# Optimization experiments

Measured on AMD Instinct MI355X. Metric: run time of the kernel, lower is better.

## Reference

```python
import jax, jax.numpy as jnp
import numpy as np

CODEBOOK_SIZE = 8192
HIDDEN_SIZE = 256
N_ANCHORS = 5


def setup_inputs() -> dict:
    key = jax.random.key(0)
    k1, k2 = jax.random.split(key)
    z = jax.random.normal(k1, (8, 4096, HIDDEN_SIZE), dtype=jnp.float32)
    emb = 0.02 * jax.random.normal(k2, (CODEBOOK_SIZE, HIDDEN_SIZE), dtype=jnp.float32)
    # enforce_anchor_values(): first 5 rows are one-hot anchors (eye padded with zeros)
    anchors = jnp.zeros((N_ANCHORS, HIDDEN_SIZE), dtype=jnp.float32)
    anchors = anchors.at[:, :N_ANCHORS].set(jnp.eye(N_ANCHORS, dtype=jnp.float32))
    emb = emb.at[:N_ANCHORS, :].set(anchors)
    return {"z": z, "emb": emb}


def reference(z, emb):
    b, t, h = z.shape
    flat = z.reshape(b * t, h)
    # squared L2 distance: ||z||^2 - 2 z.e + ||e||^2  -> [b*t, K]
    dist = (
        jnp.sum(flat * flat, axis=1, keepdims=True)
        - 2.0 * (flat @ emb.T)
        + jnp.sum(emb * emb, axis=1)[None, :]
    )
    idx = jnp.argmin(dist, axis=1)  # [b*t]
    z_q = emb[idx].reshape(b, t, h)
    # straight-through estimator
    z_st = z + jax.lax.stop_gradient(z_q - z)
    codebook_loss = jnp.mean((z_q - jax.lax.stop_gradient(z)) ** 2)
    commit_loss = jnp.mean((z - jax.lax.stop_gradient(z_q)) ** 2)
    return z_st, idx.reshape(b, t), codebook_loss, commit_loss
```

## Files before the change

### kernel.cpp

```cpp
#include <hip/hip_runtime.h>

#define HIDDEN 256
#define K_CODES 8192
#define N_TOK 32768
#define ZST_ELEMS 8388608
#define N_ANCHORS 5
#define NCH 64
#define MARGIN 8.0e-3f
#define WLS_CAP 131072
#define WLC_CAP 131072
#define EPI_BLOCKS 8192

using short8 = __attribute__((ext_vector_type(8))) short;
using f32x4  = __attribute__((ext_vector_type(4))) float;

__device__ __forceinline__ unsigned short f2bf(float f) {
    unsigned int u = __float_as_uint(f);
    return (unsigned short)((u + 0x7fffu + ((u >> 16) & 1u)) >> 16);
}

__device__ __forceinline__ void gl2lds16(const void* g, void* l) {
    __builtin_amdgcn_global_load_lds(
        (const __attribute__((address_space(1))) unsigned int*)g,
        (__attribute__((address_space(3))) unsigned int*)l, 16, 0, 0);
}

__device__ __forceinline__ unsigned long long score_key(float s, int code) {
    unsigned int u = __float_as_uint(s);
    u = (u & 0x80000000u) ? ~u : (u | 0x80000000u);
    return (((unsigned long long)u) << 32) | (unsigned int)code;
}

__global__ void prep_kernel(const float* __restrict__ emb, const float* __restrict__ z,
                            float* __restrict__ ne, float* __restrict__ zn,
                            unsigned short* __restrict__ Bh, unsigned short* __restrict__ Ah) {
#pragma clang fp contract(off)
    int gt  = blockIdx.x * 256 + threadIdx.x;
    int row = gt >> 4;
    int sub = gt & 15;
    const float* src; unsigned short* dst; float* nrm;
    if (row < K_CODES) {
        src = emb + (size_t)row * HIDDEN;
        dst = Bh  + (size_t)row * HIDDEN;
        nrm = ne + row;
    } else {
        int r2 = row - K_CODES;
        src = z  + (size_t)r2 * HIDDEN;
        dst = Ah + (size_t)r2 * HIDDEN;
        nrm = zn + r2;
    }
    const float* p = src + (sub >> 3) * 128 + (sub & 7);
    float v = p[0];
    float r = v * v;
    #pragma unroll
    for (int i = 1; i < 16; ++i) { float w = p[8 * i]; r += w * w; }
    r += __shfl_xor(r, 1, 64);
    r += __shfl_xor(r, 2, 64);
    r += __shfl_xor(r, 4, 64);
    r += __shfl_xor(r, 8, 64);
    if (sub == 0) *nrm = r;

    const float4* s4 = (const float4*)src + sub * 4;
    #pragma unroll
    for (int j = 0; j < 2; ++j) {
        float4 a = s4[2 * j];
        float4 b = s4[2 * j + 1];
        short8 h;
        h[0] = (short)f2bf(a.x); h[1] = (short)f2bf(a.y);
        h[2] = (short)f2bf(a.z); h[3] = (short)f2bf(a.w);
        h[4] = (short)f2bf(b.x); h[5] = (short)f2bf(b.y);
        h[6] = (short)f2bf(b.z); h[7] = (short)f2bf(b.w);
        *(short8*)(dst + sub * 16 + j * 8) = h;
    }
}

__global__ __launch_bounds__(512, 4) void mfma_score_kernel(
    const unsigned short* __restrict__ Ah,
    const unsigned short* __restrict__ Bh,
    const float* __restrict__ ne,
    float* __restrict__ p1, float* __restrict__ p2, unsigned short* __restrict__ piu) {

    __shared__ unsigned short Ahs[3][256 * 32];
    __shared__ unsigned short Bhs[3][128 * 32];

    const int tid  = threadIdx.x;
    const int wm   = tid >> 6;
    const int lane = tid & 63;
    const int L    = lane & 15;
    const int q    = lane >> 4;

    const int lin  = blockIdx.x;
    const int xcd  = lin & 7;
    const int s    = lin >> 3;
    const int nb   = s >> 4;
    const int m0   = (xcd * 16 + (s & 15)) * 256;
    const int n0   = nb * 128;

    f32x4 acc[2][8] = {};

    auto STAGE = [&](int kt, int buf) {
        const int k0 = kt * 32;
        #pragma unroll
        for (int r = 0; r < 2; ++r) {
            int u   = tid + 512 * r;
            int row = u >> 2;
            int p   = u & 3;
            int ch  = p ^ ((row >> 1) & 3);
            gl2lds16(Ah + (size_t)(m0 + row) * HIDDEN + k0 + ch * 8,
                     &Ahs[buf][u * 8]);
        }
        {
            int u   = tid;
            int row = u >> 2;
            int p   = u & 3;
            int ch  = p ^ ((row >> 1) & 3);
            gl2lds16(Bh + (size_t)(n0 + row) * HIDDEN + k0 + ch * 8,
                     &Bhs[buf][u * 8]);
        }
    };

    STAGE(0, 0);
    STAGE(1, 1);
    asm volatile("s_waitcnt vmcnt(3)" ::: "memory");
    __builtin_amdgcn_s_barrier();
    asm volatile("" ::: "memory");

    #pragma unroll
    for (int kt = 0; kt < 8; ++kt) {
        const int cur = kt % 3;

        const short8* A8h = (const short8*)Ahs[cur];
        const short8* B8h = (const short8*)Bhs[cur];

        short8 ah[2];
        #pragma unroll
        for (int tm = 0; tm < 2; ++tm) {
            int m  = wm * 32 + tm * 16 + L;
            ah[tm] = A8h[m * 4 + (q ^ ((m >> 1) & 3))];
        }

        if (kt + 2 < 8) STAGE(kt + 2, (kt + 2) % 3);

        __builtin_amdgcn_s_setprio(1);
        #pragma unroll
        for (int tn = 0; tn < 8; ++tn) {
            int n  = tn * 16 + L;
            short8 bh = B8h[n * 4 + (q ^ ((n >> 1) & 3))];
            #pragma unroll
            for (int tm = 0; tm < 2; ++tm) {
                acc[tm][tn] = __builtin_amdgcn_mfma_f32_16x16x32_bf16(
                    ah[tm], bh, acc[tm][tn], 0, 0, 0);
            }
        }
        __builtin_amdgcn_s_setprio(0);

        asm volatile("" ::: "memory");
        __builtin_amdgcn_s_barrier();
        if (kt < 7) {
            if (kt < 6) asm volatile("s_waitcnt vmcnt(3)" ::: "memory");
            else        asm volatile("s_waitcnt vmcnt(0)" ::: "memory");
            __builtin_amdgcn_s_barrier();
            asm volatile("" ::: "memory");
        }
    }

    float nev[8];
    #pragma unroll
    for (int tn = 0; tn < 8; ++tn) nev[tn] = ne[n0 + tn * 16 + L];
    if (nb == 0 && L < N_ANCHORS) nev[0] = 3.4e38f;

    #pragma unroll
    for (int tm = 0; tm < 2; ++tm) {
        #pragma unroll
        for (int reg = 0; reg < 4; ++reg) {
            float m1 = 3.4e38f, m2 = 3.4e38f;
            int bi = 0;
            #pragma unroll
            for (int tn = 0; tn < 8; ++tn) {
                float s2 = nev[tn] - 2.0f * acc[tm][tn][reg];
                int lo = tn * 16 + L;
                if (s2 < m1)      { m2 = m1; m1 = s2; bi = lo; }
                else if (s2 < m2) { m2 = s2; }
            }
            #pragma unroll
            for (int off = 1; off < 16; off <<= 1) {
                float o1 = __shfl_xor(m1, off, 64);
                float o2 = __shfl_xor(m2, off, 64);
                int   oi = __shfl_xor(bi, off, 64);
                if (o1 < m1 || (o1 == m1 && oi < bi)) {
                    m2 = fminf(m1, o2); m1 = o1; bi = oi;
                } else {
                    m2 = fminf(m2, o1);
                }
            }
            if (L == 0) {
                size_t mrow = (size_t)m0 + wm * 32 + tm * 16 + q * 4 + reg;
                p1[(size_t)nb * N_TOK + mrow]  = m1;
                p2[(size_t)nb * N_TOK + mrow]  = m2;
                piu[(size_t)nb * N_TOK + mrow] = (unsigned short)bi;
            }
        }
    }
}

__global__ void combine_kernel(const float* __restrict__ p1, const float* __restrict__ p2,
                               const unsigned short* __restrict__ piu,
                               const float* __restrict__ z, const float* __restrict__ zn,
                               const float* __restrict__ ne,
                               float* __restrict__ idxf, int* __restrict__ flags,
                               unsigned long long* __restrict__ slots,
                               int* __restrict__ wls, int* __restrict__ wlc,
                               unsigned int* __restrict__ wcnt) {
#pragma clang fp contract(off)
    int gt  = blockIdx.x * 256 + threadIdx.x;
    int t   = gt >> 3;
    int sub = gt & 7;

    float o1v[8], o2v[8];
    float m1 = 3.4e38f, m2 = 3.4e38f;
    int bi = 0;
    #pragma unroll
    for (int j = 0; j < 8; ++j) {
        int nb = sub + j * 8;
        float o1 = p1[(size_t)nb * N_TOK + t];
        float o2 = p2[(size_t)nb * N_TOK + t];
        o1v[j] = o1; o2v[j] = o2;
        if (o1 < m1) {
            m2 = fminf(m1, o2); m1 = o1;
            bi = nb * 128 + (int)piu[(size_t)nb * N_TOK + t];
        } else {
            m2 = fminf(m2, o1);
        }
    }
    #pragma unroll
    for (int off = 1; off < 8; off <<= 1) {
        float o1 = __shfl_xor(m1, off, 64);
        float o2 = __shfl_xor(m2, off, 64);
        int   oi = __shfl_xor(bi, off, 64);
        if (o1 < m1 || (o1 == m1 && oi < bi)) {
            m2 = fminf(m1, o2); m1 = o1; bi = oi;
        } else {
            m2 = fminf(m2, o1);
        }
    }
    float zt = zn[t];
    const float* zp = z + (size_t)t * HIDDEN;
    float sa = 3.4e38f; int ai = 0;
    #pragma unroll
    for (int a = 0; a < N_ANCHORS; ++a) {
        float s = (zt - 2.0f * zp[a]) + ne[a];
        if (s < sa) { sa = s; ai = a; }
    }
    float g = sa - zt;
    bool anchorWin = (g + MARGIN < m1);
    bool amb = !anchorWin && ((m2 - m1 < MARGIN) || (g <= m1 + MARGIN));
    if (sub == 0) {
        slots[t] = score_key(sa, ai);
        idxf[t]  = anchorWin ? (float)ai : (float)bi;
        flags[t] = amb ? 1 : 0;
    }
    if (amb) {
        float thr = m1 + MARGIN;
        #pragma unroll
        for (int j = 0; j < 8; ++j) {
            int nb = sub + j * 8;
            if (o1v[j] <= thr) {
                if (o2v[j] <= thr) {
                    unsigned int pos = atomicAdd(&wcnt[1], 2u);
                    if (pos + 1 < WLC_CAP) {
                        wlc[pos]     = (t << 7) | (nb * 2);
                        wlc[pos + 1] = (t << 7) | (nb * 2 + 1);
                    }
                } else {
                    unsigned int pos = atomicAdd(&wcnt[0], 1u);
                    if (pos < WLS_CAP)
                        wls[pos] = (t << 13) | (nb * 128 + (int)piu[(size_t)nb * N_TOK + t]);
                }
            }
        }
    }
}

__global__ __launch_bounds__(256) void rescue_fused(
    const float* __restrict__ z, const float* __restrict__ emb,
    const float* __restrict__ ne, const float* __restrict__ zn,
    const int* __restrict__ wls, const int* __restrict__ wlc,
    const unsigned int* __restrict__ wcnt,
    unsigned long long* __restrict__ slots) {
#pragma clang fp contract(off)
    int ns = (int)wcnt[0];
    if (ns > WLS_CAP) ns = WLS_CAP;
    for (int i = blockIdx.x * 256 + threadIdx.x; i < ns; i += gridDim.x * 256) {
        int it = wls[i];
        int t  = it >> 13;
        int c  = it & (K_CODES - 1);
        const float4* zp = (const float4*)(z + (size_t)t * HIDDEN);
        const float4* ep = (const float4*)(emb + (size_t)c * HIDDEN);
        float acc = 0.0f;
        #pragma unroll 8
        for (int k4 = 0; k4 < 64; ++k4) {
            float4 zv = zp[k4];
            float4 ev = ep[k4];
            acc = __builtin_fmaf(ev.x, zv.x, acc);
            acc = __builtin_fmaf(ev.y, zv.y, acc);
            acc = __builtin_fmaf(ev.z, zv.z, acc);
            acc = __builtin_fmaf(ev.w, zv.w, acc);
        }
        float s = (zn[t] - 2.0f * acc) + ne[c];
        atomicMin(&slots[t], score_key(s, c));
    }

    int nit = (int)wcnt[1];
    if (nit > WLC_CAP) nit = WLC_CAP;
    const int lane = threadIdx.x & 63;
    const int wid  = (blockIdx.x * 256 + threadIdx.x) >> 6;
    const int nw   = gridDim.x * 4;

    for (int item = wid; item < nit; item += nw) {
        int w   = wlc[item];
        int t   = w >> 7;
        int nb2 = w & 127;
        int c   = nb2 * 64 + lane;
        const float4* e4  = (const float4*)(emb + (size_t)c * HIDDEN);
        const float4* zp4 = (const float4*)(z + (size_t)t * HIDDEN);
        float acc = 0.0f;
        #pragma unroll 8
        for (int k4 = 0; k4 < 64; ++k4) {
            float4 zv = zp4[k4];
            float4 ev = e4[k4];
            acc = __builtin_fmaf(ev.x, zv.x, acc);
            acc = __builtin_fmaf(ev.y, zv.y, acc);
            acc = __builtin_fmaf(ev.z, zv.z, acc);
            acc = __builtin_fmaf(ev.w, zv.w, acc);
        }
        float t1 = zn[t] - 2.0f * acc;
        float s  = t1 + ne[c];

        unsigned long long key = score_key(s, c);
        #pragma unroll
        for (int off = 1; off < 64; off <<= 1) {
            unsigned long long o = __shfl_xor(key, off, 64);
            if (o < key) key = o;
        }
        if (lane == 0) atomicMin(&slots[t], key);
    }
}

__global__ void epilogue_kernel(const float* __restrict__ z, const float* __restrict__ emb,
                                const int* __restrict__ flags,
                                const unsigned long long* __restrict__ slots,
                                float* __restrict__ idxf, float* __restrict__ zst,
                                float* __restrict__ loss_part) {
    int t4    = blockIdx.x * 256 + threadIdx.x;
    int token = t4 >> 6;
    int k4    = t4 & 63;

    int idx;
    if (flags[token]) idx = (int)(unsigned int)(slots[token] & 0xFFFFFFFFULL);
    else              idx = (int)idxf[token];
    if (k4 == 0) idxf[token] = (float)idx;

    float4 zv = ((const float4*)z)[t4];
    float4 ev = ((const float4*)emb)[(size_t)idx * 64 + k4];

    float dx = ev.x - zv.x, dy = ev.y - zv.y, dz = ev.z - zv.z, dw = ev.w - zv.w;
    float4 o = { zv.x + dx, zv.y + dy, zv.z + dz, zv.w + dw };
    ((float4*)zst)[t4] = o;

    float p = dx * dx + dy * dy + dz * dz + dw * dw;
    #pragma unroll
    for (int off = 32; off; off >>= 1) p += __shfl_down(p, off, 64);

    __shared__ float wsum[4];
    int lane = threadIdx.x & 63, w = threadIdx.x >> 6;
    if (lane == 0) wsum[w] = p;
    __syncthreads();
    if (threadIdx.x == 0)
        loss_part[blockIdx.x] = wsum[0] + wsum[1] + wsum[2] + wsum[3];
}

__global__ __launch_bounds__(256) void finalize_kernel(
    const float* __restrict__ loss_part, float* __restrict__ out_losses) {
    float s = 0.0f;
    for (int i = threadIdx.x; i < EPI_BLOCKS; i += 256) s += loss_part[i];
    #pragma unroll
    for (int off = 32; off; off >>= 1) s += __shfl_down(s, off, 64);
    __shared__ float ws[4];
    int lane = threadIdx.x & 63, w = threadIdx.x >> 6;
    if (lane == 0) ws[w] = s;
    __syncthreads();
    if (threadIdx.x == 0) {
        float m = (ws[0] + ws[1] + ws[2] + ws[3]) * (1.0f / (float)ZST_ELEMS);
        out_losses[0] = m;
        out_losses[1] = m;
    }
}

extern "C" void kernel_launch(void* const* d_in, const int* in_sizes, int n_in,
                              void* d_out, int out_size, void* d_ws, size_t ws_size,
                              hipStream_t stream) {
    const float* z   = (const float*)d_in[0];
    const float* emb = (const float*)d_in[1];

    float* out    = (float*)d_out;
    float* zst    = out;
    float* idxf   = out + ZST_ELEMS;
    float* losses = out + ZST_ELEMS + N_TOK;

    char* w = (char*)d_ws;
    unsigned short* Ah = (unsigned short*)w;    w += (size_t)N_TOK  * HIDDEN * 2;
    unsigned short* Bh = (unsigned short*)w;    w += (size_t)K_CODES * HIDDEN * 2;
    float* p1 = (float*)w;                      w += (size_t)NCH * N_TOK * 4;
    float* p2 = (float*)w;                      w += (size_t)NCH * N_TOK * 4;
    unsigned short* piu = (unsigned short*)w;   w += (size_t)NCH * N_TOK * 2;
    float* ne = (float*)w;                      w += K_CODES * 4;
    float* zn = (float*)w;                      w += N_TOK * 4;
    int*   flags = (int*)w;                     w += N_TOK * 4;
    unsigned long long* slots = (unsigned long long*)w;  w += N_TOK * 8;
    int*   wls = (int*)w;                       w += (size_t)WLS_CAP * 4;
    int*   wlc = (int*)w;                       w += (size_t)WLC_CAP * 4;
    float* loss_part = (float*)w;               w += (size_t)EPI_BLOCKS * 4;
    unsigned int* wcnt = (unsigned int*)w;

    hipMemsetAsync(wcnt, 0, 8, stream);
    prep_kernel<<<(K_CODES + N_TOK) * 16 / 256, 256, 0, stream>>>(emb, z, ne, zn, Bh, Ah);
    mfma_score_kernel<<<N_TOK / 256 * NCH, 512, 0, stream>>>(Ah, Bh, ne, p1, p2, piu);
    combine_kernel<<<N_TOK * 8 / 256, 256, 0, stream>>>(p1, p2, piu, z, zn, ne,
                                                        idxf, flags, slots, wls, wlc, wcnt);
    rescue_fused<<<1024, 256, 0, stream>>>(z, emb, ne, zn, wls, wlc, wcnt, slots);
    epilogue_kernel<<<EPI_BLOCKS, 256, 0, stream>>>(z, emb, flags, slots,
                                                    idxf, zst, loss_part);
    finalize_kernel<<<1, 256, 0, stream>>>(loss_part, losses);
}
```

Baseline: 406.6 us.

## Fuse combine and rescue kernels with per-block LDS worklists; pack partial minima

```diff
diff --git a/kernel.cpp b/kernel.cpp
--- a/kernel.cpp
+++ b/kernel.cpp
@@ -7,9 +7,9 @@
 #define N_ANCHORS 5
 #define NCH 64
 #define MARGIN 8.0e-3f
-#define WLS_CAP 131072
-#define WLC_CAP 131072
 #define EPI_BLOCKS 8192
+#define LCAP 4096
+#define SCAP 2048
 
 using short8 = __attribute__((ext_vector_type(8))) short;
 using f32x4  = __attribute__((ext_vector_type(4))) float;
@@ -78,7 +78,7 @@
     const unsigned short* __restrict__ Ah,
     const unsigned short* __restrict__ Bh,
     const float* __restrict__ ne,
-    float* __restrict__ p1, float* __restrict__ p2, unsigned short* __restrict__ piu) {
+    float2* __restrict__ p12, unsigned short* __restrict__ piu) {
 
     __shared__ unsigned short Ahs[3][256 * 32];
     __shared__ unsigned short Bhs[3][128 * 32];
@@ -195,26 +195,31 @@
             }
             if (L == 0) {
                 size_t mrow = (size_t)m0 + wm * 32 + tm * 16 + q * 4 + reg;
-                p1[(size_t)nb * N_TOK + mrow]  = m1;
-                p2[(size_t)nb * N_TOK + mrow]  = m2;
+                p12[(size_t)nb * N_TOK + mrow] = (float2){m1, m2};
                 piu[(size_t)nb * N_TOK + mrow] = (unsigned short)bi;
             }
         }
     }
 }
 
-__global__ void combine_kernel(const float* __restrict__ p1, const float* __restrict__ p2,
-                               const unsigned short* __restrict__ piu,
-                               const float* __restrict__ z, const float* __restrict__ zn,
-                               const float* __restrict__ ne,
-                               float* __restrict__ idxf, int* __restrict__ flags,
-                               unsigned long long* __restrict__ slots,
-                               int* __restrict__ wls, int* __restrict__ wlc,
-                               unsigned int* __restrict__ wcnt) {
+__global__ __launch_bounds__(256) void combine_rescue(
+    const float2* __restrict__ p12, const unsigned short* __restrict__ piu,
+    const float* __restrict__ z, const float* __restrict__ zn,
+    const float* __restrict__ ne, const float* __restrict__ emb,
+    float* __restrict__ idxf, int* __restrict__ flags,
+    unsigned long long* __restrict__ slots) {
 #pragma clang fp contract(off)
+    __shared__ int sList[LCAP];
+    __shared__ int sSing[SCAP];
+    __shared__ unsigned int sCnt[2];
+
+    if (threadIdx.x < 2) sCnt[threadIdx.x] = 0;
+    __syncthreads();
+
     int gt  = blockIdx.x * 256 + threadIdx.x;
     int t   = gt >> 3;
     int sub = gt & 7;
+    int tl  = threadIdx.x >> 3;
 
     float o1v[8], o2v[8];
     float m1 = 3.4e38f, m2 = 3.4e38f;
@@ -222,14 +227,13 @@
     #pragma unroll
     for (int j = 0; j < 8; ++j) {
         int nb = sub + j * 8;
-        float o1 = p1[(size_t)nb * N_TOK + t];
-        float o2 = p2[(size_t)nb * N_TOK + t];
-        o1v[j] = o1; o2v[j] = o2;
-        if (o1 < m1) {
-            m2 = fminf(m1, o2); m1 = o1;
+        float2 o12 = p12[(size_t)nb * N_TOK + t];
+        o1v[j] = o12.x; o2v[j] = o12.y;
+        if (o12.x < m1) {
+            m2 = fminf(m1, o12.y); m1 = o12.x;
             bi = nb * 128 + (int)piu[(size_t)nb * N_TOK + t];
         } else {
-            m2 = fminf(m2, o1);
+            m2 = fminf(m2, o12.x);
         }
     }
     #pragma unroll
@@ -266,63 +270,51 @@
             int nb = sub + j * 8;
             if (o1v[j] <= thr) {
                 if (o2v[j] <= thr) {
-                    unsigned int pos = atomicAdd(&wcnt[1], 2u);
-                    if (pos + 1 < WLC_CAP) {
-                        wlc[pos]     = (t << 7) | (nb * 2);
-                        wlc[pos + 1] = (t << 7) | (nb * 2 + 1);
-                    }
+                    unsigned int pos = atomicAdd(&sCnt[0], 2u);
+                    sList[pos]     = (tl << 7) | (nb * 2);
+                    sList[pos + 1] = (tl << 7) | (nb * 2 + 1);
                 } else {
-                    unsigned int pos = atomicAdd(&wcnt[0], 1u);
-                    if (pos < WLS_CAP)
-                        wls[pos] = (t << 13) | (nb * 128 + (int)piu[(size_t)nb * N_TOK + t]);
+                    unsigned int pos = atomicAdd(&sCnt[1], 1u);
+                    sSing[pos] = (tl << 13) | (nb * 128 + (int)piu[(size_t)nb * N_TOK + t]);
                 }
             }
         }
     }
-}
-
-__global__ __launch_bounds__(256) void rescue_fused(
-    const float* __restrict__ z, const float* __restrict__ emb,
-    const float* __restrict__ ne, const float* __restrict__ zn,
-    const int* __restrict__ wls, const int* __restrict__ wlc,
-    const unsigned int* __restrict__ wcnt,
-    unsigned long long* __restrict__ slots) {
-#pragma clang fp contract(off)
-    int ns = (int)wcnt[0];
-    if (ns > WLS_CAP) ns = WLS_CAP;
-    for (int i = blockIdx.x * 256 + threadIdx.x; i < ns; i += gridDim.x * 256) {
-        int it = wls[i];
-        int t  = it >> 13;
+    __syncthreads();
+
+    const int nC = (int)sCnt[0];
+    const int nS = (int)sCnt[1];
+    const int tBase = blockIdx.x * 32;
+
+    for (int i = threadIdx.x; i < nS; i += 256) {
+        int it = sSing[i];
+        int t2 = tBase + (it >> 13);
         int c  = it & (K_CODES - 1);
-        const float4* zp = (const float4*)(z + (size_t)t * HIDDEN);
-        const float4* ep = (const float4*)(emb + (size_t)c * HIDDEN);
+        const float4* zp4 = (const float4*)(z + (size_t)t2 * HIDDEN);
+        const float4* ep  = (const float4*)(emb + (size_t)c * HIDDEN);
         float acc = 0.0f;
         #pragma unroll 8
         for (int k4 = 0; k4 < 64; ++k4) {
-            float4 zv = zp[k4];
+            float4 zv = zp4[k4];
             float4 ev = ep[k4];
             acc = __builtin_fmaf(ev.x, zv.x, acc);
             acc = __builtin_fmaf(ev.y, zv.y, acc);
             acc = __builtin_fmaf(ev.z, zv.z, acc);
             acc = __builtin_fmaf(ev.w, zv.w, acc);
         }
-        float s = (zn[t] - 2.0f * acc) + ne[c];
-        atomicMin(&slots[t], score_key(s, c));
-    }
-
-    int nit = (int)wcnt[1];
-    if (nit > WLC_CAP) nit = WLC_CAP;
+        float s = (zn[t2] - 2.0f * acc) + ne[c];
+        atomicMin(&slots[t2], score_key(s, c));
+    }
+
     const int lane = threadIdx.x & 63;
-    const int wid  = (blockIdx.x * 256 + threadIdx.x) >> 6;
-    const int nw   = gridDim.x * 4;
-
-    for (int item = wid; item < nit; item += nw) {
-        int w   = wlc[item];
-        int t   = w >> 7;
+    const int wv   = threadIdx.x >> 6;
+    for (int i = wv; i < nC; i += 4) {
+        int w   = sList[i];
+        int t2  = tBase + (w >> 7);
         int nb2 = w & 127;
         int c   = nb2 * 64 + lane;
         const float4* e4  = (const float4*)(emb + (size_t)c * HIDDEN);
-        const float4* zp4 = (const float4*)(z + (size_t)t * HIDDEN);
+        const float4* zp4 = (const float4*)(z + (size_t)t2 * HIDDEN);
         float acc = 0.0f;
         #pragma unroll 8
         for (int k4 = 0; k4 < 64; ++k4) {
@@ -333,7 +325,7 @@
             acc = __builtin_fmaf(ev.z, zv.z, acc);
             acc = __builtin_fmaf(ev.w, zv.w, acc);
         }
-        float t1 = zn[t] - 2.0f * acc;
+        float t1 = zn[t2] - 2.0f * acc;
         float s  = t1 + ne[c];
 
         unsigned long long key = score_key(s, c);
@@ -342,7 +334,7 @@
             unsigned long long o = __shfl_xor(key, off, 64);
             if (o < key) key = o;
         }
-        if (lane == 0) atomicMin(&slots[t], key);
+        if (lane == 0) atomicMin(&slots[t2], key);
     }
 }
 
@@ -410,24 +402,18 @@
     char* w = (char*)d_ws;
     unsigned short* Ah = (unsigned short*)w;    w += (size_t)N_TOK  * HIDDEN * 2;
     unsigned short* Bh = (unsigned short*)w;    w += (size_t)K_CODES * HIDDEN * 2;
-    float* p1 = (float*)w;                      w += (size_t)NCH * N_TOK * 4;
-    float* p2 = (float*)w;                      w += (size_t)NCH * N_TOK * 4;
+    float2* p12 = (float2*)w;                   w += (size_t)NCH * N_TOK * 8;
     unsigned short* piu = (unsigned short*)w;   w += (size_t)NCH * N_TOK * 2;
     float* ne = (float*)w;                      w += K_CODES * 4;
     float* zn = (float*)w;                      w += N_TOK * 4;
     int*   flags = (int*)w;                     w += N_TOK * 4;
     unsigned long long* slots = (unsigned long long*)w;  w += N_TOK * 8;
-    int*   wls = (int*)w;                       w += (size_t)WLS_CAP * 4;
-    int*   wlc = (int*)w;                       w += (size_t)WLC_CAP * 4;
     float* loss_part = (float*)w;               w += (size_t)EPI_BLOCKS * 4;
-    unsigned int* wcnt = (unsigned int*)w;
-
-    hipMemsetAsync(wcnt, 0, 8, stream);
+
     prep_kernel<<<(K_CODES + N_TOK) * 16 / 256, 256, 0, stream>>>(emb, z, ne, zn, Bh, Ah);
-    mfma_score_kernel<<<N_TOK / 256 * NCH, 512, 0, stream>>>(Ah, Bh, ne, p1, p2, piu);
-    combine_kernel<<<N_TOK * 8 / 256, 256, 0, stream>>>(p1, p2, piu, z, zn, ne,
-                                                        idxf, flags, slots, wls, wlc, wcnt);
-    rescue_fused<<<1024, 256, 0, stream>>>(z, emb, ne, zn, wls, wlc, wcnt, slots);
+    mfma_score_kernel<<<N_TOK / 256 * NCH, 512, 0, stream>>>(Ah, Bh, ne, p12, piu);
+    combine_rescue<<<N_TOK / 32, 256, 0, stream>>>(p12, piu, z, zn, ne, emb,
+                                                   idxf, flags, slots);
     epilogue_kernel<<<EPI_BLOCKS, 256, 0, stream>>>(z, emb, flags, slots,
                                                     idxf, zst, loss_part);
     finalize_kernel<<<1, 256, 0, stream>>>(loss_part, losses);
```

Result: faster. 360.8 us (-11.3%).
